# Kernel tuning notes

Hardware: AMD Instinct MI355X
Metric: run time of the kernel (lower is better)

The kernel has to match this reference:

```python
import jax, jax.numpy as jnp
import numpy as np

B, I, O, H = 1024, 64, 64, 32  # batch, input_size, output_size, hidden_size
NEG_SLOPE = 0.01  # nn.LeakyReLU default


def leaky(x):
    return jnp.where(x >= 0, x, NEG_SLOPE * x)


def setup_inputs() -> dict:
    key = jax.random.key(0)
    ks = jax.random.split(key, 9)
    u = lambda k, shape, b: jax.random.uniform(k, shape, jnp.float32, -b, b)
    # Per-edge tiny MLP params, stacked over [O, I] edges.
    # Linear(1,H): fan_in=1 -> bound 1.0 ; Linear(H,H)/Linear(H,1): bound 1/sqrt(H)
    bnd = 1.0 / np.sqrt(H)
    return {
        "x": jax.random.normal(ks[0], (B, I), jnp.float32),
        "W1": u(ks[1], (O, I, H), 1.0),        # Linear(1,H) weight
        "b1": u(ks[2], (O, I, H), 1.0),
        "W2": u(ks[3], (O, I, H, H), bnd),     # Linear(H,H) weight [out,in]
        "b2": u(ks[4], (O, I, H), bnd),
        "W3": u(ks[5], (O, I, H), bnd),        # Linear(H,1) weight
        "b3": u(ks[6], (O, I), bnd),
        "layer_w": jnp.ones((O, I), jnp.float32),           # layer_weight init 1.0
        "bias_w": u(ks[7], (O, I), 0.1),                     # bias_weight ~ U(-0.1,0.1)
    }


def reference(x, W1, b1, W2, b2, W3, b3, layer_w, bias_w):
    # All O*I edge MLPs evaluated as one batched computation.
    # h1[b,o,i,h] = leaky(x[b,i] * W1[o,i,h] + b1[o,i,h])
    h1 = leaky(x[:, None, :, None] * W1 + b1)                      # [B,O,I,H]
    h2 = leaky(jnp.einsum('boih,oikh->boik', h1, W2) + b2)         # [B,O,I,H]
    edge = jnp.einsum('boih,oih->boi', h2, W3) + b3                # [B,O,I]
    edge = bias_w * leaky(x)[:, None, :] + layer_w * edge          # per-edge output
    return edge.sum(axis=2)                                        # [B,O]
```

## Files before the change

### kernel.cpp

```cpp
#include <hip/hip_runtime.h>


#define H_   32
#define NI   64
#define NO   64
#define NB   1024
#define ROWS 64
#define MT   4
#define XSTR 66
#define NWAVE 4

typedef float    floatx4 __attribute__((ext_vector_type(4)));
typedef _Float16 halfx8  __attribute__((ext_vector_type(8)));
typedef _Float16 halfx2  __attribute__((ext_vector_type(2)));

union H8 { halfx8 v8; halfx2 v2[4]; unsigned int u[4]; };

__device__ inline float leaky(float v) { return fmaxf(v, 0.01f * v); }

__device__ inline unsigned int pkrtz(float a, float b) {
    return __builtin_bit_cast(unsigned int, __builtin_amdgcn_cvt_pkrtz(a, b));
}

__global__ __launch_bounds__(256, 4)
void kan_kernel(const float* __restrict__ x,  const float* __restrict__ W1,
                const float* __restrict__ b1, const float* __restrict__ W2,
                const float* __restrict__ b2, const float* __restrict__ W3,
                const float* __restrict__ b3, const float* __restrict__ lw,
                const float* __restrict__ bw, float* __restrict__ out)
{
    __shared__ unsigned int xsp[ROWS * XSTR];
    __shared__ _Float16 w1s[NI * H_];
    __shared__ _Float16 b1s[NI * H_];
    __shared__ unsigned int wbs[NI * H_];
    __shared__ float rc[ROWS];
    __shared__ float part[NWAVE][ROWS];

    const int t    = threadIdx.x;
    const int o    = blockIdx.x;
    const int row0 = blockIdx.y * ROWS;

    const float* xsrc = x + (size_t)row0 * NI;
    #pragma unroll
    for (int v = 0; v < 4; ++v) {
        int fe = (v * 256 + t) * 4;
        int r = fe >> 6, c = fe & 63;
        float4 xv = *(const float4*)(xsrc + fe);
        uint2 lo = { pkrtz(xv.x, xv.x), pkrtz(xv.y, xv.y) };
        uint2 hi = { pkrtz(xv.z, xv.z), pkrtz(xv.w, xv.w) };
        *(uint2*)(&xsp[r * XSTR + c])     = lo;
        *(uint2*)(&xsp[r * XSTR + c + 2]) = hi;
    }
    const float* w1g = W1 + (size_t)o * NI * H_;
    const float* b1g = b1 + (size_t)o * NI * H_;
    #pragma unroll
    for (int v = 0; v < 2; ++v) {
        int e = (v * 256 + t) * 4;
        float4 a = *(const float4*)(w1g + e);
        float4 c = *(const float4*)(b1g + e);
        uint2 pa = { pkrtz(a.x, a.y), pkrtz(a.z, a.w) };
        uint2 pc = { pkrtz(c.x, c.y), pkrtz(c.z, c.w) };
        *(uint2*)(w1s + e) = pa;
        *(uint2*)(b1s + e) = pc;
    }
    {
        int e = t * 8;
        float l = lw[o * NI + (e >> 5)];
        const float* w3g = W3 + (size_t)o * NI * H_ + e;
        const float* b2g = b2 + (size_t)o * NI * H_ + e;
        float4 wa = *(const float4*)(w3g), wb = *(const float4*)(w3g + 4);
        float4 ba = *(const float4*)(b2g), bb = *(const float4*)(b2g + 4);
        uint4 p0 = { pkrtz(l * wa.x, ba.x), pkrtz(l * wa.y, ba.y),
                     pkrtz(l * wa.z, ba.z), pkrtz(l * wa.w, ba.w) };
        uint4 p1 = { pkrtz(l * wb.x, bb.x), pkrtz(l * wb.y, bb.y),
                     pkrtz(l * wb.z, bb.z), pkrtz(l * wb.w, bb.w) };
        *(uint4*)(&wbs[e])     = p0;
        *(uint4*)(&wbs[e + 4]) = p1;
    }
    __syncthreads();

    const int lane = t & 63, wave = t >> 6;
    const int col  = lane & 15;
    const int kh   = lane >> 4;
    const int koff = kh * 8;
    const int i0   = wave * 16;

    const float* w2p0 = W2 + ((size_t)(o * NI + i0) * H_ + col) * H_ + koff;
    const float* w2p1 = w2p0 + 16 * H_;
    const halfx2 slope = { (_Float16)0.01f, (_Float16)0.01f };

    floatx4 pacc[MT];
    #pragma unroll
    for (int m = 0; m < MT; ++m)
        pacc[m] = floatx4{0.f, 0.f, 0.f, 0.f};

    floatx4 a0 = *(const floatx4*)(w2p0);
    floatx4 a1 = *(const floatx4*)(w2p0 + 4);
    floatx4 a2 = *(const floatx4*)(w2p1);
    floatx4 a3 = *(const floatx4*)(w2p1 + 4);

    #pragma unroll 2
    for (int ii = 0; ii < 16; ++ii) {
        const int i = i0 + ii;

        floatx4 n0, n1, n2, n3;
        if (ii < 15) {
            const float* np0 = w2p0 + (ii + 1) * (H_ * H_);
            const float* np1 = w2p1 + (ii + 1) * (H_ * H_);
            n0 = *(const floatx4*)(np0);
            n1 = *(const floatx4*)(np0 + 4);
            n2 = *(const floatx4*)(np1);
            n3 = *(const floatx4*)(np1 + 4);
        }

        H8 bf0, bf1;
        bf0.u[0] = pkrtz(a0[0], a0[1]);  bf0.u[1] = pkrtz(a0[2], a0[3]);
        bf0.u[2] = pkrtz(a1[0], a1[1]);  bf0.u[3] = pkrtz(a1[2], a1[3]);
        bf1.u[0] = pkrtz(a2[0], a2[1]);  bf1.u[1] = pkrtz(a2[2], a2[3]);
        bf1.u[2] = pkrtz(a3[0], a3[1]);  bf1.u[3] = pkrtz(a3[2], a3[3]);

        H8 w1v, b1v;
        w1v.v8 = *(const halfx8*)(w1s + i * H_ + koff);
        b1v.v8 = *(const halfx8*)(b1s + i * H_ + koff);

        halfx2 q0 = __builtin_bit_cast(halfx2, wbs[i * H_ + col]);
        halfx2 q1 = __builtin_bit_cast(halfx2, wbs[i * H_ + col + 16]);
        float w3e0 = (float)q0[0], b2c0 = (float)q0[1];
        float w3e1 = (float)q1[0], b2c1 = (float)q1[1];
        float p0 = 0.505f * w3e0, nn0 = 0.495f * w3e0;
        float p1 = 0.505f * w3e1, nn1 = 0.495f * w3e1;

        #pragma unroll
        for (int m = 0; m < MT; ++m) {
            halfx2 xx = __builtin_bit_cast(halfx2, xsp[(m * 16 + col) * XSTR + i]);
            H8 af;
            #pragma unroll
            for (int j = 0; j < 4; ++j) {
                halfx2 h = __builtin_elementwise_fma(xx, w1v.v2[j], b1v.v2[j]);
                af.v2[j] = __builtin_elementwise_max(h, h * slope);
            }
            floatx4 c0 = { b2c0, b2c0, b2c0, b2c0 };
            floatx4 c1 = { b2c1, b2c1, b2c1, b2c1 };
            c0 = __builtin_amdgcn_mfma_f32_16x16x32_f16(af.v8, bf0.v8, c0, 0, 0, 0);
            c1 = __builtin_amdgcn_mfma_f32_16x16x32_f16(af.v8, bf1.v8, c1, 0, 0, 0);
            #pragma unroll
            for (int r = 0; r < 4; ++r) {
                float acc = pacc[m][r];
                acc = fmaf(p0,  c0[r],
                      fmaf(nn0, fabsf(c0[r]),
                      fmaf(p1,  c1[r],
                      fmaf(nn1, fabsf(c1[r]), acc))));
                pacc[m][r] = acc;
            }
        }

        a0 = n0; a1 = n1; a2 = n2; a3 = n3;
    }

    #pragma unroll
    for (int m = 0; m < MT; ++m) {
        #pragma unroll
        for (int r = 0; r < 4; ++r) {
            float v = pacc[m][r];
            v += __shfl_xor(v, 1, 64);
            v += __shfl_xor(v, 2, 64);
            v += __shfl_xor(v, 4, 64);
            v += __shfl_xor(v, 8, 64);
            if (col == 0)
                part[wave][m * 16 + kh * 4 + r] = v;
        }
    }

    if (t < ROWS) {
        float s = 0.f;
        const float* bwp = bw + o * NI;
        const float* lp  = lw + o * NI;
        const float* b3p = b3 + o * NI;
        for (int i = 0; i < NI; ++i) {
            halfx2 hx = __builtin_bit_cast(halfx2, xsp[t * XSTR + i]);
            s += bwp[i] * leaky((float)hx[0]) + lp[i] * b3p[i];
        }
        rc[t] = s;
    }
    __syncthreads();

    if (t < ROWS) {
        float v = rc[t];
        #pragma unroll
        for (int w = 0; w < NWAVE; ++w) v += part[w][t];
        out[(size_t)(row0 + t) * NO + o] = v;
    }
}

extern "C" void kernel_launch(void* const* d_in, const int* in_sizes, int n_in,
                              void* d_out, int out_size, void* d_ws, size_t ws_size,
                              hipStream_t stream) {
    const float* x  = (const float*)d_in[0];
    const float* W1 = (const float*)d_in[1];
    const float* b1 = (const float*)d_in[2];
    const float* W2 = (const float*)d_in[3];
    const float* b2 = (const float*)d_in[4];
    const float* W3 = (const float*)d_in[5];
    const float* b3 = (const float*)d_in[6];
    const float* lw = (const float*)d_in[7];
    const float* bw = (const float*)d_in[8];
    float* out = (float*)d_out;

    dim3 grid(NO, NB / ROWS);
    kan_kernel<<<grid, dim3(256), 0, stream>>>(x, W1, b1, W2, b2, W3, b3, lw, bw, out);
}
```

Before: 115.5 us.

## Double waves per block, splitting input edges across eight waves

Raises the block size from 256 to 512 threads so eight waves each handle 8 input edges instead of four waves handling 16. The staging loads and the residual leaky/bias sum are spread across all threads, and the final reduction now sums per-wave partials. This aims to add more parallelism and memory-latency hiding per block. The cost is a larger final reduction and a more demanding launch-bounds occupancy target, which may limit registers per thread.

```diff
diff --git a/kernel.cpp b/kernel.cpp
--- a/kernel.cpp
+++ b/kernel.cpp
@@ -8,7 +8,8 @@
 #define ROWS 64
 #define MT   4
 #define XSTR 66
-#define NWAVE 4
+#define NWAVE 8
+#define ISL  8
 
 typedef float    floatx4 __attribute__((ext_vector_type(4)));
 typedef _Float16 halfx8  __attribute__((ext_vector_type(8)));
@@ -22,7 +23,7 @@
     return __builtin_bit_cast(unsigned int, __builtin_amdgcn_cvt_pkrtz(a, b));
 }
 
-__global__ __launch_bounds__(256, 4)
+__global__ __launch_bounds__(512, 8)
 void kan_kernel(const float* __restrict__ x,  const float* __restrict__ W1,
                 const float* __restrict__ b1, const float* __restrict__ W2,
                 const float* __restrict__ b2, const float* __restrict__ W3,
@@ -33,7 +34,7 @@
     __shared__ _Float16 w1s[NI * H_];
     __shared__ _Float16 b1s[NI * H_];
     __shared__ unsigned int wbs[NI * H_];
-    __shared__ float rc[ROWS];
+    __shared__ float rcs[NWAVE][ROWS];
     __shared__ float part[NWAVE][ROWS];
 
     const int t    = threadIdx.x;
@@ -42,8 +43,8 @@
 
     const float* xsrc = x + (size_t)row0 * NI;
     #pragma unroll
-    for (int v = 0; v < 4; ++v) {
-        int fe = (v * 256 + t) * 4;
+    for (int v = 0; v < 2; ++v) {
+        int fe = (v * 512 + t) * 4;
         int r = fe >> 6, c = fe & 63;
         float4 xv = *(const float4*)(xsrc + fe);
         uint2 lo = { pkrtz(xv.x, xv.x), pkrtz(xv.y, xv.y) };
@@ -53,9 +54,8 @@
     }
     const float* w1g = W1 + (size_t)o * NI * H_;
     const float* b1g = b1 + (size_t)o * NI * H_;
-    #pragma unroll
-    for (int v = 0; v < 2; ++v) {
-        int e = (v * 256 + t) * 4;
+    {
+        int e = t * 4;
         float4 a = *(const float4*)(w1g + e);
         float4 c = *(const float4*)(b1g + e);
         uint2 pa = { pkrtz(a.x, a.y), pkrtz(a.z, a.w) };
@@ -64,18 +64,15 @@
         *(uint2*)(b1s + e) = pc;
     }
     {
-        int e = t * 8;
+        int e = t * 4;
         float l = lw[o * NI + (e >> 5)];
         const float* w3g = W3 + (size_t)o * NI * H_ + e;
         const float* b2g = b2 + (size_t)o * NI * H_ + e;
-        float4 wa = *(const float4*)(w3g), wb = *(const float4*)(w3g + 4);
-        float4 ba = *(const float4*)(b2g), bb = *(const float4*)(b2g + 4);
+        float4 wa = *(const float4*)(w3g);
+        float4 ba = *(const float4*)(b2g);
         uint4 p0 = { pkrtz(l * wa.x, ba.x), pkrtz(l * wa.y, ba.y),
                      pkrtz(l * wa.z, ba.z), pkrtz(l * wa.w, ba.w) };
-        uint4 p1 = { pkrtz(l * wb.x, bb.x), pkrtz(l * wb.y, bb.y),
-                     pkrtz(l * wb.z, bb.z), pkrtz(l * wb.w, bb.w) };
-        *(uint4*)(&wbs[e])     = p0;
-        *(uint4*)(&wbs[e + 4]) = p1;
+        *(uint4*)(&wbs[e]) = p0;
     }
     __syncthreads();
 
@@ -83,7 +80,7 @@
     const int col  = lane & 15;
     const int kh   = lane >> 4;
     const int koff = kh * 8;
-    const int i0   = wave * 16;
+    const int i0   = wave * ISL;
 
     const float* w2p0 = W2 + ((size_t)(o * NI + i0) * H_ + col) * H_ + koff;
     const float* w2p1 = w2p0 + 16 * H_;
@@ -100,11 +97,11 @@
     floatx4 a3 = *(const floatx4*)(w2p1 + 4);
 
     #pragma unroll 2
-    for (int ii = 0; ii < 16; ++ii) {
+    for (int ii = 0; ii < ISL; ++ii) {
         const int i = i0 + ii;
 
         floatx4 n0, n1, n2, n3;
-        if (ii < 15) {
+        if (ii < ISL - 1) {
             const float* np0 = w2p0 + (ii + 1) * (H_ * H_);
             const float* np1 = w2p1 + (ii + 1) * (H_ * H_);
             n0 = *(const floatx4*)(np0);
@@ -171,23 +168,26 @@
         }
     }
 
-    if (t < ROWS) {
+    {
+        const int row = t & 63, seg = t >> 6;
         float s = 0.f;
         const float* bwp = bw + o * NI;
         const float* lp  = lw + o * NI;
         const float* b3p = b3 + o * NI;
-        for (int i = 0; i < NI; ++i) {
-            halfx2 hx = __builtin_bit_cast(halfx2, xsp[t * XSTR + i]);
+        #pragma unroll
+        for (int u = 0; u < NI / NWAVE; ++u) {
+            int i = seg * (NI / NWAVE) + u;
+            halfx2 hx = __builtin_bit_cast(halfx2, xsp[row * XSTR + i]);
             s += bwp[i] * leaky((float)hx[0]) + lp[i] * b3p[i];
         }
-        rc[t] = s;
+        rcs[seg][row] = s;
     }
     __syncthreads();
 
     if (t < ROWS) {
-        float v = rc[t];
-        #pragma unroll
-        for (int w = 0; w < NWAVE; ++w) v += part[w][t];
+        float v = 0.f;
+        #pragma unroll
+        for (int w = 0; w < NWAVE; ++w) v += part[w][t] + rcs[w][t];
         out[(size_t)(row0 + t) * NO + o] = v;
     }
 }
@@ -207,5 +207,5 @@
     float* out = (float*)d_out;
 
     dim3 grid(NO, NB / ROWS);
-    kan_kernel<<<grid, dim3(256), 0, stream>>>(x, W1, b1, W2, b2, W3, b3, lw, bw, out);
+    kan_kernel<<<grid, dim3(512), 0, stream>>>(x, W1, b1, W2, b2, W3, b3, lw, bw, out);
 }
```

Measured after the change: 201.1 us. 1.74x slower.
